# Performance work log

Measured on AMD Instinct MI355X. Metric: run time of the kernel, lower is better.

## Reference

```python
import jax, jax.numpy as jnp
import numpy as np

B, C_IN, H, W = 8, 3, 256, 256
CH = 64          # encoder_channels
MSG_LEN = 30     # message_length
WM_R = 4         # watermark_radius
LP_R = 50        # low-pass filter radius


def _wm_positions(h, w, c, r, msg_len):
    # Replicates the nested-loop index ordering of apply_tree_ring_watermark.
    cy, cx = h // 2, w // 2
    ch, rr, cc = [], [], []
    idx = 0
    for chan in range(c):
        for i in range(-r, r + 1):
            for j in range(-r, r + 1):
                if idx >= msg_len:
                    break
                if not (0 <= cy + i < h and 0 <= cx + j < w):
                    continue
                if (i * i + j * j) ** 0.5 <= r:
                    ch.append(chan); rr.append(cy + i); cc.append(cx + j)
                    idx += 1
    return (np.asarray(ch, np.int32), np.asarray(rr, np.int32), np.asarray(cc, np.int32))

_WM_CH, _WM_ROW, _WM_COL = _wm_positions(H, W, CH, WM_R, MSG_LEN)


def conv2d(x, w, b, pad):
    y = jax.lax.conv_general_dilated(x, w, (1, 1), [(pad, pad), (pad, pad)],
                                     dimension_numbers=('NCHW', 'OIHW', 'NCHW'))
    return y + b[None, :, None, None]


def conv_bn_relu(x, w, b, g, be):
    y = conv2d(x, w, b, 1)
    m = y.mean(axis=(0, 2, 3), keepdims=True)
    v = y.var(axis=(0, 2, 3), keepdims=True)
    y = (y - m) * jax.lax.rsqrt(v + 1e-5) * g[None, :, None, None] + be[None, :, None, None]
    return jax.nn.relu(y)


def low_pass_filter(image, radius=LP_R):
    # np.fft per-channel low pass with a circular mask (cv2.circle disk), clip+uint8, /255.
    h, w = image.shape[-2:]
    yy = jnp.arange(h, dtype=jnp.float32) - h // 2
    xx = jnp.arange(w, dtype=jnp.float32) - w // 2
    mask = (yy[:, None] ** 2 + xx[None, :] ** 2) <= float(radius * radius)
    f = jnp.fft.fftshift(jnp.fft.fft2(image), axes=(-2, -1))
    low = jnp.fft.ifft2(jnp.fft.ifftshift(f * mask, axes=(-2, -1))).real
    low = jnp.floor(jnp.clip(low, 0.0, 255.0)) / 255.0  # uint8 cast = floor for non-neg
    # torch version detaches to CPU numpy -> no gradient through this path
    return jax.lax.stop_gradient(low.astype(image.dtype))


def apply_tree_ring_watermark(image_fft, message):
    # Vectorized replacement of the quadruple nested loop: fixed static scatter positions.
    vals = jax.lax.stop_gradient(message).astype(image_fft.dtype) * (1.0 + 1.0j)  # [B, L]
    return image_fft.at[:, _WM_CH, _WM_ROW, _WM_COL].set(vals)


def setup_inputs() -> dict:
    key = jax.random.key(0)
    ks = jax.random.split(key, 8)
    s = 0.05
    return {
        'image': jax.random.uniform(ks[0], (B, C_IN, H, W), jnp.float32) * 255.0,
        'message': jax.random.randint(ks[1], (B, MSG_LEN), 0, 2).astype(jnp.float32),
        'w0': jax.random.normal(ks[2], (CH, C_IN, 3, 3), jnp.float32) * s,
        'b0': jnp.zeros((CH,), jnp.float32),
        'g0': jnp.ones((CH,), jnp.float32),
        'be0': jnp.zeros((CH,), jnp.float32),
        'ws': jax.random.normal(ks[3], (3, CH, CH, 3, 3), jnp.float32) * s,
        'bs': jnp.zeros((3, CH), jnp.float32),
        'gs': jnp.ones((3, CH), jnp.float32),
        'bes': jnp.zeros((3, CH), jnp.float32),
        'acw': jax.random.normal(ks[4], (CH, CH + C_IN + MSG_LEN, 3, 3), jnp.float32) * s,
        'acb': jnp.zeros((CH,), jnp.float32),
        'acg': jnp.ones((CH,), jnp.float32),
        'acbe': jnp.zeros((CH,), jnp.float32),
        'fw': jax.random.normal(ks[5], (3, CH, 1, 1), jnp.float32) * s,
        'fb': jnp.zeros((3,), jnp.float32),
    }


def reference(image, message, w0, b0, g0, be0, ws, bs, gs, bes,
              acw, acb, acg, acbe, fw, fb):
    lp = low_pass_filter(image)
    x = conv_bn_relu(lp, w0, b0, g0, be0)
    for k in range(3):  # encoder_blocks - 1
        x = conv_bn_relu(x, ws[k], bs[k], gs[k], bes[k])
    f = jnp.fft.fft2(x)
    f = apply_tree_ring_watermark(f, message)
    enc = jnp.fft.ifft2(f).real
    msg_exp = jnp.broadcast_to(message[:, :, None, None], (B, MSG_LEN, H, W))
    concat = jnp.concatenate([msg_exp, enc, image], axis=1)
    y = conv_bn_relu(concat, acw, acb, acg, acbe)
    return conv2d(y, fw, fb, 0)
```

## Files before the change

kernel.cpp:

```cpp
#include <hip/hip_runtime.h>
#include <math.h>


#define NPX 65536
typedef unsigned short u16;
typedef __bf16 bfrag_t __attribute__((ext_vector_type(8)));
typedef float f32x4 __attribute__((ext_vector_type(4)));

__constant__ int WM_R_[30] = {124, 125,125,125,125,125, 126,126,126,126,126,126,126,
                              127,127,127,127,127,127,127,
                              128,128,128,128,128,128,128,128,128, 129};
__constant__ int WM_C_[30] = {128, 126,127,128,129,130, 125,126,127,128,129,130,131,
                              125,126,127,128,129,130,131,
                              124,125,126,127,128,129,130,131,132, 125};

__device__ __forceinline__ float bfu2f(unsigned int bits) {
    return __uint_as_float(bits << 16);
}
__device__ __forceinline__ u16 f2bu(float f) {
    unsigned int u = __float_as_uint(f);
    u += 0x7fffu + ((u >> 16) & 1u);
    return (u16)(u >> 16);
}
__device__ __forceinline__ unsigned cvt_pk(float lo, float hi) {
    unsigned r;
    asm("v_cvt_pk_bf16_f32 %0, %1, %2" : "=v"(r) : "v"(lo), "v"(hi));
    return r;
}

__global__ void k_tables(float* __restrict__ tw, float* __restrict__ d2t,
                         double* __restrict__ twd64) {
    int idx = blockIdx.x * 256 + threadIdx.x;
    if (idx < 256) {
        double ang = -2.0 * M_PI * (double)idx / 256.0;
        tw[idx]       = (float)cos(ang);
        tw[256 + idx] = (float)sin(ang);
        twd64[idx]       = cos(ang);
        twd64[256 + idx] = sin(ang);
    }
    int q = idx - 256;
    if (q >= 0 && q < 256 * 101) {
        int d = q / 101, kxi = q - d * 101;
        int vx = (kxi <= 50) ? kxi : kxi - 101;
        int r2 = 2500 - vx * vx;
        int L = 0;
        while ((L + 1) * (L + 1) <= r2) L++;
        double s = 1.0;
        for (int v = 1; v <= L; v++) s += 2.0 * cos(2.0 * M_PI * (double)(v * d) / 256.0);
        d2t[kxi * 256 + d] = (float)(s / 256.0);
    }
}

__global__ __launch_bounds__(256) void k_lp1(const float* __restrict__ img,
        const double* __restrict__ twd64, float* __restrict__ Y) {
    __shared__ double rowd[4][256];
    int y0 = blockIdx.x * 4, ch = blockIdx.y, tid = threadIdx.x;
#pragma unroll
    for (int r = 0; r < 4; r++)
        rowd[r][tid] = (double)img[ch * NPX + (y0 + r) * 256 + tid];
    __syncthreads();
    int kxi = tid & 127, rg = tid >> 7;
    if (kxi >= 101) return;
    int kx = (kxi <= 50) ? kxi : kxi + 155;
    double cr = twd64[kx], ci = twd64[256 + kx];
    double wr = 1.0, wi = 0.0;
    double a0r = 0, a0i = 0, a1r = 0, a1i = 0;
    const double* r0 = rowd[2 * rg];
    const double* r1 = rowd[2 * rg + 1];
    for (int x = 0; x < 256; x++) {
        double v0 = r0[x], v1 = r1[x];
        a0r += v0 * wr; a0i += v0 * wi;
        a1r += v1 * wr; a1i += v1 * wi;
        double t = wr * cr - wi * ci;
        wi = wr * ci + wi * cr;
        wr = t;
    }
    int y = y0 + 2 * rg;
    int o = ((kxi * 24 + ch) * 256 + y) * 2;
    Y[o]     = (float)a0r; Y[o + 1] = (float)a0i;
    Y[o + 2] = (float)a1r; Y[o + 3] = (float)a1i;
}

__global__ __launch_bounds__(256) void k_lp2(const float* __restrict__ Y,
        const float* __restrict__ d2t, float* __restrict__ W) {
    __shared__ double Ys[4][256][2];
    __shared__ double Dc[256];
    int kxi = blockIdx.x, chg = blockIdx.y, tid = threadIdx.x;
    const float* src = Y + (size_t)(kxi * 24 + chg * 4) * 512;
    double* ysf = (double*)Ys;
    for (int i = tid; i < 2048; i += 256) ysf[i] = (double)src[i];
    Dc[tid] = (double)d2t[kxi * 256 + tid];
    __syncthreads();
    int cs = tid >> 6, y4 = tid & 63;
    double wr[4] = {0, 0, 0, 0}, wi[4] = {0, 0, 0, 0};
    for (int yp = 0; yp < 256; yp++) {
        double yr = Ys[cs][yp][0], yi = Ys[cs][yp][1];
        double D0 = Dc[(y4 - yp) & 255];
        double D1 = Dc[(y4 + 64 - yp) & 255];
        double D2 = Dc[(y4 + 128 - yp) & 255];
        double D3 = Dc[(y4 + 192 - yp) & 255];
        wr[0] += D0 * yr; wi[0] += D0 * yi;
        wr[1] += D1 * yr; wi[1] += D1 * yi;
        wr[2] += D2 * yr; wi[2] += D2 * yi;
        wr[3] += D3 * yr; wi[3] += D3 * yi;
    }
    int ch = chg * 4 + cs;
#pragma unroll
    for (int k = 0; k < 4; k++) {
        int y = y4 + 64 * k;
        int o = ((ch * 256 + y) * 101 + kxi) * 2;
        W[o] = (float)wr[k]; W[o + 1] = (float)wi[k];
    }
}

__global__ __launch_bounds__(256) void k_lp3(const float* __restrict__ W,
        const double* __restrict__ twd64, float* __restrict__ lp) {
    __shared__ double wsr[101], wsi[101];
    int y = blockIdx.x, ch = blockIdx.y, x = threadIdx.x;
    if (x < 101) {
        int kxi = (x < 50) ? (x + 51) : (x - 50);
        wsr[x] = (double)W[((ch * 256 + y) * 101 + kxi) * 2];
        wsi[x] = (double)W[((ch * 256 + y) * 101 + kxi) * 2 + 1];
    }
    __syncthreads();
    int t0 = (50 * x) & 255;
    double wr = twd64[t0], wi = -twd64[256 + t0];
    double cr = twd64[x], ci = twd64[256 + x];
    double acc = 0.0;
    for (int j = 0; j < 101; j++) {
        acc += wsr[j] * wr + wsi[j] * wi;
        double t = wr * cr - wi * ci;
        wi = wr * ci + wi * cr;
        wr = t;
    }
    acc *= (1.0 / 256.0);
    acc = floor(fmin(fmax(acc, 0.0), 255.0)) / 255.0;
    lp[ch * NPX + y * 256 + x] = (float)acc;
}

__global__ __launch_bounds__(256, 2) void k_conv1(
    const float* __restrict__ lp, const float* __restrict__ w0,
    u16* __restrict__ out, float* __restrict__ part) {
    __shared__ float wl[3][9][64];
    __shared__ float al[3][18][18];
    int tid = threadIdx.x;
    int b = blockIdx.z, r0 = blockIdx.y * 16, c0 = blockIdx.x * 16;
    int ocg = tid >> 5, pxg = tid & 31;
    int row = pxg >> 1, chof = (pxg & 1) * 8;
    int oc0 = ocg * 8;
    float acc[8][8];
#pragma unroll
    for (int o = 0; o < 8; o++)
#pragma unroll
        for (int p = 0; p < 8; p++) acc[o][p] = 0.f;
    for (int idx = tid; idx < 1728; idx += 256) {
        int ic = idx / 576, rem = idx - ic * 576;
        int tap = rem >> 6, oc = rem & 63;
        wl[ic][tap][oc] = w0[(oc * 3 + ic) * 9 + tap];
    }
    for (int idx = tid; idx < 972; idx += 256) {
        int ic = idx / 324, rem = idx - ic * 324;
        int ly = rem / 18, lx = rem - ly * 18;
        int gy = r0 - 1 + ly, gx = c0 - 1 + lx;
        float v = 0.f;
        if ((unsigned)gy < 256u && (unsigned)gx < 256u)
            v = lp[(b * 3 + ic) * NPX + gy * 256 + gx];
        al[ic][ly][lx] = v;
    }
    __syncthreads();
    for (int ic = 0; ic < 3; ic++) {
        float areg[3][10];
#pragma unroll
        for (int di = 0; di < 3; di++)
#pragma unroll
            for (int xx = 0; xx < 10; xx++) areg[di][xx] = al[ic][row + di][chof + xx];
#pragma unroll
        for (int tap = 0; tap < 9; tap++) {
            const int di = tap / 3, dj = tap % 3;
            float wv[8];
#pragma unroll
            for (int o = 0; o < 8; o++) wv[o] = wl[ic][tap][oc0 + o];
#pragma unroll
            for (int o = 0; o < 8; o++)
#pragma unroll
                for (int p = 0; p < 8; p++)
                    acc[o][p] = fmaf(wv[o], areg[di][dj + p], acc[o][p]);
        }
    }
    float es1[8], es2[8];
#pragma unroll
    for (int o = 0; o < 8; o++) { es1[o] = 0.f; es2[o] = 0.f; }
#pragma unroll
    for (int p = 0; p < 8; p++) {
        unsigned wd[4];
#pragma unroll
        for (int q = 0; q < 4; q++)
            wd[q] = cvt_pk(acc[2 * q][p], acc[2 * q + 1][p]);
#pragma unroll
        for (int o = 0; o < 8; o++) {
            float v = acc[o][p];
            es1[o] += v; es2[o] += v * v;
        }
        size_t addr = ((size_t)((b * 256 + r0 + row) * 256 + c0 + chof + p)) * 64 + oc0;
        uint4 vv; vv.x = wd[0]; vv.y = wd[1]; vv.z = wd[2]; vv.w = wd[3];
        *reinterpret_cast<uint4*>(out + addr) = vv;
    }
#pragma unroll
    for (int m = 1; m < 32; m <<= 1) {
#pragma unroll
        for (int o = 0; o < 8; o++) {
            es1[o] += __shfl_xor(es1[o], m);
            es2[o] += __shfl_xor(es2[o], m);
        }
    }
    if ((tid & 31) == 0) {
        int slot = (blockIdx.x + 16 * (blockIdx.y + 16 * blockIdx.z)) & 63;
        float* pp = part + slot * 128;
#pragma unroll
        for (int o = 0; o < 8; o++) {
            atomicAdd(&pp[(oc0 + o) * 2],     es1[o]);
            atomicAdd(&pp[(oc0 + o) * 2 + 1], es2[o]);
        }
    }
}

__global__ void k_wprep(const float* __restrict__ wsv, u16* __restrict__ wp) {
    int bid = blockIdx.x;
    int conv = bid / 72, fg = bid % 72;
    int icc = fg / 36, t2 = fg % 36, tap = t2 / 4, ocb = t2 % 4;
    int l = threadIdx.x;
    int oc = ocb * 16 + (l & 15);
    unsigned wd[4];
#pragma unroll
    for (int q = 0; q < 4; q++) {
        int ic0 = icc * 32 + (l >> 4) * 8 + 2 * q;
        float v0 = wsv[conv * 36864 + (oc * 64 + ic0) * 9 + tap];
        float v1 = wsv[conv * 36864 + (oc * 64 + ic0 + 1) * 9 + tap];
        wd[q] = (unsigned)f2bu(v0) | ((unsigned)f2bu(v1) << 16);
    }
    uint4 vv; vv.x = wd[0]; vv.y = wd[1]; vv.z = wd[2]; vv.w = wd[3];
    reinterpret_cast<uint4*>(wp)[conv * 4608 + fg * 64 + l] = vv;
}

__global__ void k_wprep5(const float* __restrict__ acw, u16* __restrict__ wp5) {
    int fg = blockIdx.x;
    int icc = fg / 36, t2 = fg % 36, tap = t2 / 4, ocb = t2 % 4;
    int l = threadIdx.x;
    int oc = ocb * 16 + (l & 15);
    unsigned wd[4];
#pragma unroll
    for (int q = 0; q < 4; q++) {
        unsigned out2 = 0;
#pragma unroll
        for (int h = 0; h < 2; h++) {
            int icp = icc * 32 + (l >> 4) * 8 + 2 * q + h;
            float v = 0.f;
            if (icp < 67) v = acw[(oc * 97 + 30 + icp) * 9 + tap];
            out2 |= ((unsigned)f2bu(v)) << (16 * h);
        }
        wd[q] = out2;
    }
    uint4 vv; vv.x = wd[0]; vv.y = wd[1]; vv.z = wd[2]; vv.w = wd[3];
    reinterpret_cast<uint4*>(wp5)[fg * 64 + l] = vv;
}

__global__ void k_wsum(const float* __restrict__ acw, float* __restrict__ wsum) {
    for (int e = threadIdx.x; e < 17280; e += 256) {
        int oc = e / 270, r2 = e % 270, ic = r2 / 9, cls = r2 % 9;
        int cy = cls / 3, cx = cls % 3;
        int dil = (cy == 0) ? 1 : 0, dih = (cy == 2) ? 1 : 2;
        int djl = (cx == 0) ? 1 : 0, djh = (cx == 2) ? 1 : 2;
        float s = 0.f;
        for (int di = dil; di <= dih; di++)
            for (int dj = djl; dj <= djh; dj++)
                s += acw[(oc * 97 + ic) * 9 + di * 3 + dj];
        wsum[e] = s;
    }
}

__global__ void k_msgM(const float* __restrict__ msg, const float* __restrict__ wsum,
                       float* __restrict__ M) {
    int b = blockIdx.x;
    for (int t = threadIdx.x; t < 576; t += 256) {
        int oc = t / 9, cls = t % 9;
        float s = 0.f;
        for (int ic = 0; ic < 30; ic++)
            s += msg[b * 30 + ic] * wsum[oc * 270 + ic * 9 + cls];
        M[b * 576 + t] = s;
    }
}

template <int MODE>
__global__ __launch_bounds__(256, 3) void k_cmfma(
    const u16* __restrict__ src, const u16* __restrict__ wp,
    const float* __restrict__ st, const float* __restrict__ img,
    const float* __restrict__ dlt, const float* __restrict__ tw,
    const float* __restrict__ Mterm, u16* __restrict__ out,
    float* __restrict__ part) {
    const int NKB = (MODE == 0) ? 8 : 9;
    __shared__ __align__(16) u16 ain[NKB * 324 * 8];
    __shared__ float sst[128];
    __shared__ float aux[512];
    __shared__ float dl[(MODE == 1) ? 60 : 1];
    __shared__ float Ml[(MODE == 1) ? 576 : 1];

    int tid = threadIdx.x;
    int wv = tid >> 6, l = tid & 63;
    int b = blockIdx.z, y0 = blockIdx.y * 16, x0 = blockIdx.x * 16;

    if (tid < 128) sst[tid] = st[tid];
    if (MODE == 1) {
        aux[tid] = tw[tid]; aux[tid + 256] = tw[tid + 256];
        if (tid < 60) dl[tid] = dlt[b * 60 + tid];
        for (int i = tid; i < 576; i += 256) Ml[i] = Mterm[b * 576 + i];
    }
    __syncthreads();

    for (int px = tid; px < 324; px += 256) {
        int ly = px / 18, lx = px - ly * 18;
        int gy = y0 - 1 + ly, gx = x0 - 1 + lx;
        bool inb = ((unsigned)gy < 256u) && ((unsigned)gx < 256u);
        uint4* dst = reinterpret_cast<uint4*>(ain) + px;
        const uint4* gp = nullptr;
        if (inb) gp = reinterpret_cast<const uint4*>(
            src + ((size_t)((b * 256 + gy) * 256 + gx)) * 64);
        float corr = 0.f;
        if (MODE == 1 && inb) {
#pragma unroll
            for (int p = 0; p < 30; p++) {
                int t = (WM_R_[p] * gy + WM_C_[p] * gx) & 255;
                corr += dl[2 * p] * aux[t] + dl[2 * p + 1] * aux[256 + t];
            }
            corr *= (1.0f / 65536.0f);
        }
#pragma unroll
        for (int kb = 0; kb < 8; kb++) {
            uint4 pk; pk.x = 0; pk.y = 0; pk.z = 0; pk.w = 0;
            if (inb) {
                uint4 u = gp[kb];
                int cb = kb * 8;
                float f0 = fmaxf(bfu2f(u.x & 0xffffu) * sst[2 * cb + 0]  + sst[2 * cb + 1],  0.f);
                float f1 = fmaxf(bfu2f(u.x >> 16)     * sst[2 * cb + 2]  + sst[2 * cb + 3],  0.f);
                float f2 = fmaxf(bfu2f(u.y & 0xffffu) * sst[2 * cb + 4]  + sst[2 * cb + 5],  0.f);
                float f3 = fmaxf(bfu2f(u.y >> 16)     * sst[2 * cb + 6]  + sst[2 * cb + 7],  0.f);
                float f4 = fmaxf(bfu2f(u.z & 0xffffu) * sst[2 * cb + 8]  + sst[2 * cb + 9],  0.f);
                float f5 = fmaxf(bfu2f(u.z >> 16)     * sst[2 * cb + 10] + sst[2 * cb + 11], 0.f);
                float f6 = fmaxf(bfu2f(u.w & 0xffffu) * sst[2 * cb + 12] + sst[2 * cb + 13], 0.f);
                float f7 = fmaxf(bfu2f(u.w >> 16)     * sst[2 * cb + 14] + sst[2 * cb + 15], 0.f);
                if (MODE == 1 && kb == 0) f0 += corr;
                pk.x = cvt_pk(f0, f1); pk.y = cvt_pk(f2, f3);
                pk.z = cvt_pk(f4, f5); pk.w = cvt_pk(f6, f7);
            }
            dst[kb * 324] = pk;
        }
        if (MODE == 1) {
            uint4 p8; p8.x = 0; p8.y = 0; p8.z = 0; p8.w = 0;
            if (inb) {
                float v0 = img[(b * 3 + 0) * NPX + gy * 256 + gx];
                float v1 = img[(b * 3 + 1) * NPX + gy * 256 + gx];
                float v2 = img[(b * 3 + 2) * NPX + gy * 256 + gx];
                p8.x = cvt_pk(v0, v1);
                p8.y = cvt_pk(v2, 0.f);
            }
            dst[8 * 324] = p8;
        }
    }
    __syncthreads();

    f32x4 acc[4][4];
#pragma unroll
    for (int nt = 0; nt < 4; nt++)
#pragma unroll
        for (int ob = 0; ob < 4; ob++) acc[nt][ob] = (f32x4)(0.f);

    const uint4* wq = reinterpret_cast<const uint4*>(wp);
    const uint4* ap = reinterpret_cast<const uint4*>(ain);
    const int bl = (l >> 4) * 324 + (l & 15);
    const int wv4 = wv * 4;
    const int NIT = (MODE == 0) ? 18 : 27;

    uint4 a0 = wq[l], a1 = wq[64 + l], a2 = wq[128 + l], a3 = wq[192 + l];
#pragma unroll 1
    for (int it = 0; it < NIT; it++) {
        uint4 n0, n1, n2, n3;
        if (it + 1 < NIT) {
            const uint4* q = wq + (it + 1) * 256 + l;
            n0 = q[0]; n1 = q[64]; n2 = q[128]; n3 = q[192];
        }
        int icc = it / 9, tap = it - icc * 9;
        int di = tap / 3, dj = tap - di * 3;
        int abase = (MODE == 1 && icc == 2) ? (8 * 324 + (l & 15) + dj)
                                            : (icc * 4 * 324 + bl + dj);
#pragma unroll
        for (int nt = 0; nt < 4; nt++) {
            uint4 braw = ap[abase + (wv4 + nt + di) * 18];
            bfrag_t bf = __builtin_bit_cast(bfrag_t, braw);
            acc[nt][0] = __builtin_amdgcn_mfma_f32_16x16x32_bf16(
                __builtin_bit_cast(bfrag_t, a0), bf, acc[nt][0], 0, 0, 0);
            acc[nt][1] = __builtin_amdgcn_mfma_f32_16x16x32_bf16(
                __builtin_bit_cast(bfrag_t, a1), bf, acc[nt][1], 0, 0, 0);
            acc[nt][2] = __builtin_amdgcn_mfma_f32_16x16x32_bf16(
                __builtin_bit_cast(bfrag_t, a2), bf, acc[nt][2], 0, 0, 0);
            acc[nt][3] = __builtin_amdgcn_mfma_f32_16x16x32_bf16(
                __builtin_bit_cast(bfrag_t, a3), bf, acc[nt][3], 0, 0, 0);
        }
        a0 = n0; a1 = n1; a2 = n2; a3 = n3;
    }

    int x = x0 + (l & 15);
    int ocq = (l >> 4) * 4;
    int clsx = (x == 0) ? 0 : ((x == 255) ? 2 : 1);
    float es1[16], es2[16];
#pragma unroll
    for (int k = 0; k < 16; k++) { es1[k] = 0.f; es2[k] = 0.f; }
#pragma unroll
    for (int nt = 0; nt < 4; nt++) {
        int y = y0 + wv4 + nt;
#pragma unroll
        for (int ob = 0; ob < 4; ob++) {
            int oc = ob * 16 + ocq;
            float v0 = acc[nt][ob][0], v1 = acc[nt][ob][1];
            float v2 = acc[nt][ob][2], v3 = acc[nt][ob][3];
            if (MODE == 1) {
                int cls = ((y == 0) ? 0 : ((y == 255) ? 6 : 3)) + clsx;
                v0 += Ml[(oc + 0) * 9 + cls];
                v1 += Ml[(oc + 1) * 9 + cls];
                v2 += Ml[(oc + 2) * 9 + cls];
                v3 += Ml[(oc + 3) * 9 + cls];
            }
            es1[ob * 4 + 0] += v0; es2[ob * 4 + 0] += v0 * v0;
            es1[ob * 4 + 1] += v1; es2[ob * 4 + 1] += v1 * v1;
            es1[ob * 4 + 2] += v2; es2[ob * 4 + 2] += v2 * v2;
            es1[ob * 4 + 3] += v3; es2[ob * 4 + 3] += v3 * v3;
            uint2 pk;
            pk.x = cvt_pk(v0, v1);
            pk.y = cvt_pk(v2, v3);
            size_t addr = ((size_t)((b * 256 + y) * 256 + x)) * 64 + oc;
            *reinterpret_cast<uint2*>(out + addr) = pk;
        }
    }
#pragma unroll
    for (int m = 1; m < 16; m <<= 1) {
#pragma unroll
        for (int k = 0; k < 16; k++) {
            es1[k] += __shfl_xor(es1[k], m);
            es2[k] += __shfl_xor(es2[k], m);
        }
    }
    __syncthreads();
    if ((l & 15) == 0) {
#pragma unroll
        for (int k = 0; k < 16; k++) {
            int ob = k >> 2, q = k & 3;
            int oc = ob * 16 + ocq + q;
            aux[wv * 128 + oc * 2]     = es1[k];
            aux[wv * 128 + oc * 2 + 1] = es2[k];
        }
    }
    __syncthreads();
    if (tid < 128) {
        float v = aux[tid] + aux[128 + tid] + aux[256 + tid] + aux[384 + tid];
        int slot = (blockIdx.x + 16 * (blockIdx.y + 16 * blockIdx.z)) & 63;
        atomicAdd(&part[slot * 128 + tid], v);
    }
}

__global__ void k_finalize(float* __restrict__ part, const float* __restrict__ g,
                           const float* __restrict__ be, float* __restrict__ st) {
    int c = threadIdx.x;
    double S1 = 0.0, S2 = 0.0;
    for (int k = 0; k < 64; k++) {
        S1 += (double)part[k * 128 + c * 2];
        S2 += (double)part[k * 128 + c * 2 + 1];
    }
    const double Nn = 524288.0;
    double mean = S1 / Nn;
    double var = S2 / Nn - mean * mean;
    float s = (float)((double)g[c] / sqrt(var + 1e-5));
    float t = (float)((double)be[c] - mean * (double)s);
    __syncthreads();
    for (int k = c; k < 8192; k += 64) part[k] = 0.f;
    st[c * 2] = s; st[c * 2 + 1] = t;
}

__global__ void k_wmG(const u16* __restrict__ y4, const float* __restrict__ st,
                      const float* __restrict__ tw, float* __restrict__ G) {
    __shared__ float twl[512];
    __shared__ float red[256][12];
    int b = blockIdx.x, xg = blockIdx.y, tid = threadIdx.x;
    twl[tid] = tw[tid]; twl[tid + 256] = tw[tid + 256];
    __syncthreads();
    int xs = tid & 31, x = xg * 32 + xs, yg = tid >> 5;
    float s0 = st[0], t0 = st[1];
    float gr[6], gi[6];
#pragma unroll
    for (int r = 0; r < 6; r++) { gr[r] = 0.f; gi[r] = 0.f; }
    for (int yy = 0; yy < 32; yy++) {
        int y = yg * 32 + yy;
        float v = fmaxf(bfu2f((unsigned)y4[((size_t)((b * 256 + y) * 256 + x)) * 64]) * s0 + t0, 0.f);
#pragma unroll
        for (int r = 0; r < 6; r++) {
            int t = ((124 + r) * y) & 255;
            gr[r] += v * twl[t];
            gi[r] += v * twl[256 + t];
        }
    }
#pragma unroll
    for (int r = 0; r < 6; r++) { red[tid][2 * r] = gr[r]; red[tid][2 * r + 1] = gi[r]; }
    __syncthreads();
    for (int e = tid; e < 384; e += 256) {
        int xs2 = e & 31, c = e >> 5;
        float s = 0.f;
        for (int g = 0; g < 8; g++) s += red[g * 32 + xs2][c];
        int r = c >> 1, ri = c & 1;
        G[((b * 6 + r) * 256 + (xg * 32 + xs2)) * 2 + ri] = s;
    }
}

__global__ void k_wmC(const float* __restrict__ G, const float* __restrict__ msg,
                      const float* __restrict__ tw, float* __restrict__ dlt) {
    __shared__ float twl[512];
    __shared__ float fr[256], fi[256];
    int b = blockIdx.x, tid = threadIdx.x;
    twl[tid] = tw[tid]; twl[tid + 256] = tw[tid + 256];
    __syncthreads();
    int p = tid >> 3, part = tid & 7;
    float Fr = 0.f, Fi = 0.f;
    if (p < 30) {
        int rp = WM_R_[p] - 124, c = WM_C_[p];
        for (int xx = part * 32; xx < part * 32 + 32; xx++) {
            float gr = G[((b * 6 + rp) * 256 + xx) * 2];
            float gi = G[((b * 6 + rp) * 256 + xx) * 2 + 1];
            int u = (c * xx) & 255;
            Fr += gr * twl[u] - gi * twl[256 + u];
            Fi += gr * twl[256 + u] + gi * twl[u];
        }
    }
    fr[tid] = Fr; fi[tid] = Fi;
    __syncthreads();
    if (p < 30 && part == 0) {
        float sr = 0.f, si = 0.f;
        for (int k = 0; k < 8; k++) { sr += fr[p * 8 + k]; si += fi[p * 8 + k]; }
        float m = msg[b * 30 + p];
        dlt[b * 60 + p * 2]     = m - sr;
        dlt[b * 60 + p * 2 + 1] = m - si;
    }
}

__global__ void k_final(const u16* __restrict__ y5, const float* __restrict__ st,
                        const float* __restrict__ fw, const float* __restrict__ fb,
                        float* __restrict__ out) {
    __shared__ float fwl[192];
    __shared__ float sl[64], tl[64];
    __shared__ float fbl[3];
    int tid = threadIdx.x;
    if (tid < 192) fwl[tid] = fw[tid];
    if (tid < 64) { sl[tid] = st[tid * 2]; tl[tid] = st[tid * 2 + 1]; }
    if (tid < 3) fbl[tid] = fb[tid];
    __syncthreads();
    int e = blockIdx.x * 256 + tid;
    int b = e >> 16, px = e & 65535;
    float a0 = fbl[0], a1 = fbl[1], a2 = fbl[2];
    const u16* rowp = y5 + (size_t)e * 64;
    for (int cb = 0; cb < 8; cb++) {
        uint4 u = *reinterpret_cast<const uint4*>(rowp + cb * 8);
        unsigned wd[4] = {u.x, u.y, u.z, u.w};
#pragma unroll
        for (int q = 0; q < 4; q++) {
            int c = cb * 8 + 2 * q;
            float v0 = fmaxf(bfu2f(wd[q] & 0xffffu) * sl[c] + tl[c], 0.f);
            float v1 = fmaxf(bfu2f(wd[q] >> 16) * sl[c + 1] + tl[c + 1], 0.f);
            a0 += v0 * fwl[c] + v1 * fwl[c + 1];
            a1 += v0 * fwl[64 + c] + v1 * fwl[64 + c + 1];
            a2 += v0 * fwl[128 + c] + v1 * fwl[128 + c + 1];
        }
    }
    out[(b * 3 + 0) * NPX + px] = a0;
    out[(b * 3 + 1) * NPX + px] = a1;
    out[(b * 3 + 2) * NPX + px] = a2;
}

extern "C" void kernel_launch(void* const* d_in, const int* in_sizes, int n_in,
                              void* d_out, int out_size, void* d_ws, size_t ws_size,
                              hipStream_t stream) {
    (void)in_sizes; (void)n_in; (void)out_size; (void)ws_size;
    const float* image   = (const float*)d_in[0];
    const float* message = (const float*)d_in[1];
    const float* w0      = (const float*)d_in[2];
    const float* g0      = (const float*)d_in[4];
    const float* be0     = (const float*)d_in[5];
    const float* wsv     = (const float*)d_in[6];
    const float* gs      = (const float*)d_in[8];
    const float* bes     = (const float*)d_in[9];
    const float* acw     = (const float*)d_in[10];
    const float* acg     = (const float*)d_in[12];
    const float* acbe    = (const float*)d_in[13];
    const float* fw      = (const float*)d_in[14];
    const float* fb      = (const float*)d_in[15];
    float* out = (float*)d_out;

    u16* XA   = (u16*)d_ws;
    u16* XB   = XA + 33554432;
    float* Yb = (float*)XB;
    float* Wb = Yb + 1241088;
    float* LP = Wb + 1241088;
    u16* WPa  = XB + 33554432;
    u16* WP5  = WPa + 110592;
    float* TW   = (float*)(WP5 + 55296);
    float* D2T  = TW + 512;
    float* PART = D2T + 25856;
    float* ST   = PART + 32768;
    float* DLT  = ST + 128;
    float* G    = DLT + 480;
    float* WSm  = G + 24576;
    float* Mt   = WSm + 17280;
    double* TW64 = (double*)(Mt + 4608);

    dim3 cgrid(16, 16, 8);

    hipMemsetAsync(PART, 0, 32768, stream);
    k_tables<<<103, 256, 0, stream>>>(TW, D2T, TW64);
    k_wprep<<<216, 64, 0, stream>>>(wsv, WPa);
    k_wprep5<<<108, 64, 0, stream>>>(acw, WP5);
    k_wsum<<<1, 256, 0, stream>>>(acw, WSm);
    k_msgM<<<8, 256, 0, stream>>>(message, WSm, Mt);

    k_lp1<<<dim3(64, 24), 256, 0, stream>>>(image, TW64, Yb);
    k_lp2<<<dim3(101, 6), 256, 0, stream>>>(Yb, D2T, Wb);
    k_lp3<<<dim3(256, 24), 256, 0, stream>>>(Wb, TW64, LP);

    k_conv1<<<cgrid, 256, 0, stream>>>(LP, w0, XA, PART);
    k_finalize<<<1, 64, 0, stream>>>(PART, g0, be0, ST);
    k_cmfma<0><<<cgrid, 256, 0, stream>>>(XA, WPa + 0 * 36864, ST, nullptr, nullptr, nullptr, nullptr, XB, PART);
    k_finalize<<<1, 64, 0, stream>>>(PART, gs + 0, bes + 0, ST);
    k_cmfma<0><<<cgrid, 256, 0, stream>>>(XB, WPa + 1 * 36864, ST, nullptr, nullptr, nullptr, nullptr, XA, PART);
    k_finalize<<<1, 64, 0, stream>>>(PART, gs + 64, bes + 64, ST);
    k_cmfma<0><<<cgrid, 256, 0, stream>>>(XA, WPa + 2 * 36864, ST, nullptr, nullptr, nullptr, nullptr, XB, PART);
    k_finalize<<<1, 64, 0, stream>>>(PART, gs + 128, bes + 128, ST);
    k_wmG<<<dim3(8, 8), 256, 0, stream>>>(XB, ST, TW, G);
    k_wmC<<<8, 256, 0, stream>>>(G, message, TW, DLT);
    k_cmfma<1><<<cgrid, 256, 0, stream>>>(XB, WP5, ST, image, DLT, TW, Mt, XA, PART);
    k_finalize<<<1, 64, 0, stream>>>(PART, acg, acbe, ST);
    k_final<<<2048, 256, 0, stream>>>(XA, ST, fw, fb, out);
}
```

Measured before the change: 702.2 us.

## Replace atomic BN partial sums with per-block stores and swizzle block order

Each conv block now writes its BN sum and sum-of-squares partials to its own slot instead of atomically adding into 64 shared slots. This removes the memset and the zeroing inside finalize. Finalize becomes a 1024-thread single block that reduces all 2048 per-block partials in double. Block indices are also swizzled so consecutive workgroups map to different batches, which changes cache/XCD locality. The trade is that finalize now reads far more partial data on a single CU five times.

```diff
diff --git a/kernel.cpp b/kernel.cpp
--- a/kernel.cpp
+++ b/kernel.cpp
@@ -144,7 +144,9 @@
     __shared__ float wl[3][9][64];
     __shared__ float al[3][18][18];
     int tid = threadIdx.x;
-    int b = blockIdx.z, r0 = blockIdx.y * 16, c0 = blockIdx.x * 16;
+    int lin = blockIdx.x + 16 * (blockIdx.y + 16 * blockIdx.z);
+    int swz = (lin & 7) * 256 + (lin >> 3);
+    int b = swz >> 8, r0 = ((swz >> 4) & 15) * 16, c0 = (swz & 15) * 16;
     int ocg = tid >> 5, pxg = tid & 31;
     int row = pxg >> 1, chof = (pxg & 1) * 8;
     int oc0 = ocg * 8;
@@ -214,12 +216,11 @@
         }
     }
     if ((tid & 31) == 0) {
-        int slot = (blockIdx.x + 16 * (blockIdx.y + 16 * blockIdx.z)) & 63;
-        float* pp = part + slot * 128;
+        float* pp = part + (size_t)swz * 128;
 #pragma unroll
         for (int o = 0; o < 8; o++) {
-            atomicAdd(&pp[(oc0 + o) * 2],     es1[o]);
-            atomicAdd(&pp[(oc0 + o) * 2 + 1], es2[o]);
+            pp[(oc0 + o) * 2]     = es1[o];
+            pp[(oc0 + o) * 2 + 1] = es2[o];
         }
     }
 }
@@ -306,7 +307,9 @@
 
     int tid = threadIdx.x;
     int wv = tid >> 6, l = tid & 63;
-    int b = blockIdx.z, y0 = blockIdx.y * 16, x0 = blockIdx.x * 16;
+    int lin = blockIdx.x + 16 * (blockIdx.y + 16 * blockIdx.z);
+    int swz = (lin & 7) * 256 + (lin >> 3);
+    int b = swz >> 8, y0 = ((swz >> 4) & 15) * 16, x0 = (swz & 15) * 16;
 
     if (tid < 128) sst[tid] = st[tid];
     if (MODE == 1) {
@@ -460,27 +463,37 @@
     __syncthreads();
     if (tid < 128) {
         float v = aux[tid] + aux[128 + tid] + aux[256 + tid] + aux[384 + tid];
-        int slot = (blockIdx.x + 16 * (blockIdx.y + 16 * blockIdx.z)) & 63;
-        atomicAdd(&part[slot * 128 + tid], v);
-    }
-}
-
-__global__ void k_finalize(float* __restrict__ part, const float* __restrict__ g,
-                           const float* __restrict__ be, float* __restrict__ st) {
-    int c = threadIdx.x;
-    double S1 = 0.0, S2 = 0.0;
-    for (int k = 0; k < 64; k++) {
-        S1 += (double)part[k * 128 + c * 2];
-        S2 += (double)part[k * 128 + c * 2 + 1];
-    }
-    const double Nn = 524288.0;
-    double mean = S1 / Nn;
-    double var = S2 / Nn - mean * mean;
-    float s = (float)((double)g[c] / sqrt(var + 1e-5));
-    float t = (float)((double)be[c] - mean * (double)s);
-    __syncthreads();
-    for (int k = c; k < 8192; k += 64) part[k] = 0.f;
-    st[c * 2] = s; st[c * 2 + 1] = t;
+        part[(size_t)swz * 128 + tid] = v;
+    }
+}
+
+__global__ __launch_bounds__(1024) void k_finalize(const float* __restrict__ part,
+        const float* __restrict__ g, const float* __restrict__ be,
+        float* __restrict__ st) {
+    __shared__ double red[8][128];
+    int tid = threadIdx.x;
+    int pos = tid & 127, grp = tid >> 7;
+    double s = 0.0;
+    const float* p = part + (size_t)grp * 256 * 128 + pos;
+    for (int k = 0; k < 256; k++) s += (double)p[k * 128];
+    red[grp][pos] = s;
+    __syncthreads();
+    if (tid < 128) {
+        double T = 0.0;
+#pragma unroll
+        for (int gq = 0; gq < 8; gq++) T += red[gq][tid];
+        red[0][tid] = T;
+    }
+    __syncthreads();
+    if (tid < 64) {
+        double S1 = red[0][tid * 2], S2 = red[0][tid * 2 + 1];
+        const double Nn = 524288.0;
+        double mean = S1 / Nn;
+        double var = S2 / Nn - mean * mean;
+        float sc = (float)((double)g[tid] / sqrt(var + 1e-5));
+        float tr = (float)((double)be[tid] - mean * (double)sc);
+        st[tid * 2] = sc; st[tid * 2 + 1] = tr;
+    }
 }
 
 __global__ void k_wmG(const u16* __restrict__ y4, const float* __restrict__ st,
@@ -608,17 +621,17 @@
     u16* WP5  = WPa + 110592;
     float* TW   = (float*)(WP5 + 55296);
     float* D2T  = TW + 512;
-    float* PART = D2T + 25856;
-    float* ST   = PART + 32768;
+    float* OLDP = D2T + 25856;
+    float* ST   = OLDP + 32768;
     float* DLT  = ST + 128;
     float* G    = DLT + 480;
     float* WSm  = G + 24576;
     float* Mt   = WSm + 17280;
     double* TW64 = (double*)(Mt + 4608);
+    float* PART2 = (float*)(TW64 + 512);
 
     dim3 cgrid(16, 16, 8);
 
-    hipMemsetAsync(PART, 0, 32768, stream);
     k_tables<<<103, 256, 0, stream>>>(TW, D2T, TW64);
     k_wprep<<<216, 64, 0, stream>>>(wsv, WPa);
     k_wprep5<<<108, 64, 0, stream>>>(acw, WP5);
@@ -629,17 +642,17 @@
     k_lp2<<<dim3(101, 6), 256, 0, stream>>>(Yb, D2T, Wb);
     k_lp3<<<dim3(256, 24), 256, 0, stream>>>(Wb, TW64, LP);
 
-    k_conv1<<<cgrid, 256, 0, stream>>>(LP, w0, XA, PART);
-    k_finalize<<<1, 64, 0, stream>>>(PART, g0, be0, ST);
-    k_cmfma<0><<<cgrid, 256, 0, stream>>>(XA, WPa + 0 * 36864, ST, nullptr, nullptr, nullptr, nullptr, XB, PART);
-    k_finalize<<<1, 64, 0, stream>>>(PART, gs + 0, bes + 0, ST);
-    k_cmfma<0><<<cgrid, 256, 0, stream>>>(XB, WPa + 1 * 36864, ST, nullptr, nullptr, nullptr, nullptr, XA, PART);
-    k_finalize<<<1, 64, 0, stream>>>(PART, gs + 64, bes + 64, ST);
-    k_cmfma<0><<<cgrid, 256, 0, stream>>>(XA, WPa + 2 * 36864, ST, nullptr, nullptr, nullptr, nullptr, XB, PART);
-    k_finalize<<<1, 64, 0, stream>>>(PART, gs + 128, bes + 128, ST);
+    k_conv1<<<cgrid, 256, 0, stream>>>(LP, w0, XA, PART2);
+    k_finalize<<<1, 1024, 0, stream>>>(PART2, g0, be0, ST);
+    k_cmfma<0><<<cgrid, 256, 0, stream>>>(XA, WPa + 0 * 36864, ST, nullptr, nullptr, nullptr, nullptr, XB, PART2);
+    k_finalize<<<1, 1024, 0, stream>>>(PART2, gs + 0, bes + 0, ST);
+    k_cmfma<0><<<cgrid, 256, 0, stream>>>(XB, WPa + 1 * 36864, ST, nullptr, nullptr, nullptr, nullptr, XA, PART2);
+    k_finalize<<<1, 1024, 0, stream>>>(PART2, gs + 64, bes + 64, ST);
+    k_cmfma<0><<<cgrid, 256, 0, stream>>>(XA, WPa + 2 * 36864, ST, nullptr, nullptr, nullptr, nullptr, XB, PART2);
+    k_finalize<<<1, 1024, 0, stream>>>(PART2, gs + 128, bes + 128, ST);
     k_wmG<<<dim3(8, 8), 256, 0, stream>>>(XB, ST, TW, G);
     k_wmC<<<8, 256, 0, stream>>>(G, message, TW, DLT);
-    k_cmfma<1><<<cgrid, 256, 0, stream>>>(XB, WP5, ST, image, DLT, TW, Mt, XA, PART);
-    k_finalize<<<1, 64, 0, stream>>>(PART, acg, acbe, ST);
+    k_cmfma<1><<<cgrid, 256, 0, stream>>>(XB, WP5, ST, image, DLT, TW, Mt, XA, PART2);
+    k_finalize<<<1, 1024, 0, stream>>>(PART2, acg, acbe, ST);
     k_final<<<2048, 256, 0, stream>>>(XA, ST, fw, fb, out);
 }
```

After: 724.5 us. 3.2% more time.
